# Kernel tuning notes

Hardware: AMD Instinct MI355X
Metric: run time of the kernel (lower is better)

The kernel has to match this reference:

```python
import jax, jax.numpy as jnp
import numpy as np

N = 100000      # n_entities + n_users (graph nodes)
E = 1600000     # edges
R = 8           # relations
D = 64          # entity_dim
DR = 64         # relation_dim
EPS = 1e-12


def setup_inputs() -> dict:
    key = jax.random.key(0)
    ks = jax.random.split(key, 16)
    inp = {
        'entity_emb': jax.random.normal(ks[0], (N, D), jnp.float32) * 0.1,
        'rel_emb':    jax.random.normal(ks[1], (R, DR), jnp.float32) * 0.1,
        'W_R':        jax.random.normal(ks[2], (R, D, DR), jnp.float32) * 0.1,
        'W1_0': jax.random.normal(ks[3], (32, 64), jnp.float32) * 0.1,
        'b1_0': jax.random.normal(ks[4], (32,), jnp.float32) * 0.1,
        'W2_0': jax.random.normal(ks[5], (32, 64), jnp.float32) * 0.1,
        'b2_0': jax.random.normal(ks[6], (32,), jnp.float32) * 0.1,
        'W1_1': jax.random.normal(ks[7], (16, 32), jnp.float32) * 0.1,
        'b1_1': jax.random.normal(ks[8], (16,), jnp.float32) * 0.1,
        'W2_1': jax.random.normal(ks[9], (16, 32), jnp.float32) * 0.1,
        'b2_1': jax.random.normal(ks[10], (16,), jnp.float32) * 0.1,
        'src':   jax.random.randint(ks[11], (E,), 0, N, dtype=jnp.int32),
        'dst':   jax.random.randint(ks[12], (E,), 0, N, dtype=jnp.int32),
        'etype': jax.random.randint(ks[13], (E,), 0, R, dtype=jnp.int32),
    }
    return inp


def _l2_normalize(x):
    # F.normalize(x, p=2, dim=1)
    n = jnp.linalg.norm(x, axis=1, keepdims=True)
    return x / jnp.maximum(n, EPS)


def reference(entity_emb, rel_emb, W_R, W1_0, b1_0, W2_0, b2_0,
              W1_1, b1_1, W2_1, b2_1, src, dst, etype):
    # ---- compute_attention: per-edge relation-specific projection ----
    # proj[n, r, :] = entity_emb[n] @ W_R[r]   -> [N, R, DR]
    proj = jnp.einsum('nd,rdk->nrk', entity_emb, W_R)
    r_mul_t = proj[src, etype]          # [E, DR] (edges.src)
    r_mul_h = proj[dst, etype]          # [E, DR] (edges.dst)
    r_e = rel_emb[etype]                # [E, DR]
    att = jnp.sum(r_mul_t * jnp.tanh(r_mul_h + r_e), axis=-1)  # [E]

    # ---- edge_softmax: normalize over incoming edges of each dst ----
    m = jax.ops.segment_max(att, dst, num_segments=N)           # [N]
    ex = jnp.exp(att - m[dst])
    s = jax.ops.segment_sum(ex, dst, num_segments=N)            # [N]
    a = ex / s[dst]                                             # [E]

    # ---- bi-interaction aggregator layers ----
    def agg_layer(x, W1, b1, W2, b2):
        msg = x[src] * a[:, None]                               # u_mul_e
        Nh = jax.ops.segment_sum(msg, dst, num_segments=N)      # sum to dst
        out1 = jax.nn.leaky_relu(jnp.matmul(x + Nh, W1.T) + b1, 0.01)
        out2 = jax.nn.leaky_relu(jnp.matmul(x * Nh, W2.T) + b2, 0.01)
        return _l2_normalize(out1 + out2)

    ego = entity_emb
    h1 = agg_layer(ego, W1_0, b1_0, W2_0, b2_0)   # [N, 32]
    h2 = agg_layer(h1, W1_1, b1_1, W2_1, b2_1)    # [N, 16]
    all_embed = jnp.concatenate([ego, h1, h2], axis=1)  # [N, 112]
    return all_embed
```

## Files before the change

### kernel.cpp

```cpp
#include <hip/hip_runtime.h>
#include <hip/hip_bf16.h>
#include <math.h>

#define NN 100000
#define NE 1600000
#define NR 8
#define DD 64
#define DDR 64

typedef __attribute__((ext_vector_type(8))) short bf8v;
typedef __attribute__((ext_vector_type(4))) float f4v;

__device__ __forceinline__ unsigned enc_f(float f) {
    unsigned u = __float_as_uint(f);
    return (u & 0x80000000u) ? ~u : (u | 0x80000000u);
}
__device__ __forceinline__ float dec_f(unsigned u) {
    return (u & 0x80000000u) ? __uint_as_float(u & 0x7FFFFFFFu) : __uint_as_float(~u);
}
__device__ __forceinline__ float bfs2f(unsigned short u) { return __uint_as_float(((unsigned)u) << 16); }
__device__ __forceinline__ short f2bfs(float x) {
    __hip_bfloat16 h = __float2bfloat16(x);
    return *reinterpret_cast<short*>(&h);
}
__device__ __forceinline__ unsigned pack2bf(short a, short b) {
    return (unsigned)(unsigned short)a | ((unsigned)(unsigned short)b << 16);
}
__device__ __forceinline__ float tanh_fast(float x) {
    x = fminf(fmaxf(x, -15.f), 15.f);
    float e = __expf(2.f * x);
    return (e - 1.f) * __builtin_amdgcn_rcpf(e + 1.f);
}

__global__ void __launch_bounds__(256)
k_projm(const float* __restrict__ emb, const float* __restrict__ WR,
        const float* __restrict__ rel,
        unsigned short* __restrict__ tproj, unsigned* __restrict__ embh)
{
    int t = threadIdx.x;
    int wv = t >> 6, l = t & 63;
    int lo = l & 15, hi = l >> 4;
    int r = blockIdx.y;
    int colbase = (wv & 1) * 32;
    int nwbase = blockIdx.x * 128 + (wv >> 1) * 64;

    const float* __restrict__ wb = WR + (long)r * (DD * DDR) + (hi * 8) * DDR + colbase + lo;
    bf8v B00, B01, B10, B11;
#pragma unroll
    for (int j = 0; j < 8; ++j) {
        B00[j] = f2bfs(wb[(0 * 32 + j) * DDR + 0]);
        B01[j] = f2bfs(wb[(1 * 32 + j) * DDR + 0]);
        B10[j] = f2bfs(wb[(0 * 32 + j) * DDR + 16]);
        B11[j] = f2bfs(wb[(1 * 32 + j) * DDR + 16]);
    }
    float rv0 = rel[r * DDR + colbase + lo];
    float rv1 = rel[r * DDR + colbase + lo + 16];

    for (int nt = 0; nt < 4; ++nt) {
        int nb = nwbase + nt * 16;
        int arow = nb + lo;
        float4 xa0 = make_float4(0.f, 0.f, 0.f, 0.f), xa1 = xa0, xb0 = xa0, xb1 = xa0;
        if (arow < NN) {
            const float* __restrict__ xr = emb + (long)arow * DD + hi * 8;
            xa0 = *(const float4*)(xr);
            xa1 = *(const float4*)(xr + 4);
            xb0 = *(const float4*)(xr + 32);
            xb1 = *(const float4*)(xr + 36);
        }
        bf8v A0, A1;
        A0[0] = f2bfs(xa0.x); A0[1] = f2bfs(xa0.y); A0[2] = f2bfs(xa0.z); A0[3] = f2bfs(xa0.w);
        A0[4] = f2bfs(xa1.x); A0[5] = f2bfs(xa1.y); A0[6] = f2bfs(xa1.z); A0[7] = f2bfs(xa1.w);
        A1[0] = f2bfs(xb0.x); A1[1] = f2bfs(xb0.y); A1[2] = f2bfs(xb0.z); A1[3] = f2bfs(xb0.w);
        A1[4] = f2bfs(xb1.x); A1[5] = f2bfs(xb1.y); A1[6] = f2bfs(xb1.z); A1[7] = f2bfs(xb1.w);

        if (r == 0 && arow < NN) {
            unsigned* er = embh + (long)arow * 32 + hi * 4;
            er[0]  = pack2bf(A0[0], A0[1]); er[1]  = pack2bf(A0[2], A0[3]);
            er[2]  = pack2bf(A0[4], A0[5]); er[3]  = pack2bf(A0[6], A0[7]);
            er[16] = pack2bf(A1[0], A1[1]); er[17] = pack2bf(A1[2], A1[3]);
            er[18] = pack2bf(A1[4], A1[5]); er[19] = pack2bf(A1[6], A1[7]);
        }

        f4v acc0 = {0.f, 0.f, 0.f, 0.f}, acc1 = {0.f, 0.f, 0.f, 0.f};
        acc0 = __builtin_amdgcn_mfma_f32_16x16x32_bf16(A0, B00, acc0, 0, 0, 0);
        acc0 = __builtin_amdgcn_mfma_f32_16x16x32_bf16(A1, B01, acc0, 0, 0, 0);
        acc1 = __builtin_amdgcn_mfma_f32_16x16x32_bf16(A0, B10, acc1, 0, 0, 0);
        acc1 = __builtin_amdgcn_mfma_f32_16x16x32_bf16(A1, B11, acc1, 0, 0, 0);

#pragma unroll
        for (int i = 0; i < 4; ++i) {
            int rr = nb + hi * 4 + i;
            if (rr < NN) {
                long obase = ((long)r * NN + rr) * DDR + colbase + lo;
                tproj[obase]      = (unsigned short)f2bfs(tanh_fast(acc0[i] + rv0));
                tproj[obase + 16] = (unsigned short)f2bfs(tanh_fast(acc1[i] + rv1));
            }
        }
    }
}

__global__ void __launch_bounds__(256)
k_projw2(const unsigned short* __restrict__ tproj, const float* __restrict__ WR,
         unsigned short* __restrict__ w2h)
{
    int t = threadIdx.x;
    int wv = t >> 6, l = t & 63;
    int lo = l & 15, hi = l >> 4;
    int r = blockIdx.y;
    int colbase = (wv & 1) * 32;
    int nwbase = blockIdx.x * 128 + (wv >> 1) * 64;

    const float* __restrict__ wb0 = WR + (long)r * (DD * DDR) + (long)(colbase + lo) * DDR + hi * 8;
    const float* __restrict__ wb1 = wb0 + 16 * DDR;
    bf8v B00, B01, B10, B11;
#pragma unroll
    for (int j = 0; j < 8; ++j) {
        B00[j] = f2bfs(wb0[j]);
        B01[j] = f2bfs(wb0[32 + j]);
        B10[j] = f2bfs(wb1[j]);
        B11[j] = f2bfs(wb1[32 + j]);
    }

    for (int nt = 0; nt < 4; ++nt) {
        int nb = nwbase + nt * 16;
        int arow = nb + lo;
        bf8v A0, A1;
#pragma unroll
        for (int j = 0; j < 8; ++j) { A0[j] = 0; A1[j] = 0; }
        if (arow < NN) {
            const unsigned short* ar = tproj + ((long)r * NN + arow) * DDR + hi * 8;
            A0 = *(const bf8v*)(ar);
            A1 = *(const bf8v*)(ar + 32);
        }
        f4v acc0 = {0.f, 0.f, 0.f, 0.f}, acc1 = {0.f, 0.f, 0.f, 0.f};
        acc0 = __builtin_amdgcn_mfma_f32_16x16x32_bf16(A0, B00, acc0, 0, 0, 0);
        acc0 = __builtin_amdgcn_mfma_f32_16x16x32_bf16(A1, B01, acc0, 0, 0, 0);
        acc1 = __builtin_amdgcn_mfma_f32_16x16x32_bf16(A0, B10, acc1, 0, 0, 0);
        acc1 = __builtin_amdgcn_mfma_f32_16x16x32_bf16(A1, B11, acc1, 0, 0, 0);
#pragma unroll
        for (int i = 0; i < 4; ++i) {
            int rr = nb + hi * 4 + i;
            if (rr < NN) {
                long obase = ((long)r * NN + rr) * DDR + colbase + lo;
                w2h[obase]      = (unsigned short)f2bfs(acc0[i]);
                w2h[obase + 16] = (unsigned short)f2bfs(acc1[i]);
            }
        }
    }
}

__global__ void k_hist(const int* __restrict__ dst, unsigned* __restrict__ cnt)
{
    int e = blockIdx.x * blockDim.x + threadIdx.x;
    if (e >= NE) return;
    atomicAdd(cnt + dst[e], 1u);
}

__global__ void k_base(const unsigned* __restrict__ cnt, unsigned* __restrict__ gcur,
                       unsigned* __restrict__ base, unsigned* __restrict__ curs)
{
    int i = blockIdx.x * blockDim.x + threadIdx.x;
    int lane = threadIdx.x & 63;
    unsigned v = (i < NN) ? cnt[i] : 0u;
    unsigned p = v;
#pragma unroll
    for (int off = 1; off < 64; off <<= 1) {
        unsigned q = __shfl_up(p, off);
        if (lane >= off) p += q;
    }
    unsigned tot = __shfl(p, 63);
    unsigned gb = 0;
    if (lane == 0) gb = atomicAdd(gcur, tot);
    gb = __shfl(gb, 0);
    if (i < NN) {
        unsigned b = gb + p - v;
        base[i] = b;
        curs[i] = b;
    }
}

__global__ void k_scatter2(const int* __restrict__ dst, const int* __restrict__ src,
                           const int* __restrict__ et, unsigned* __restrict__ curs,
                           unsigned* __restrict__ srcet)
{
    int e = blockIdx.x * blockDim.x + threadIdx.x;
    if (e >= NE) return;
    unsigned pos = atomicAdd(curs + dst[e], 1u);
    srcet[pos] = (unsigned)src[e] | ((unsigned)et[e] << 28);
}

__global__ void __launch_bounds__(256)
k_mega0w(const float* __restrict__ emb, const unsigned short* __restrict__ embh,
         const unsigned short* __restrict__ w2h,
         const unsigned* __restrict__ cnt, const unsigned* __restrict__ basep,
         const unsigned* __restrict__ srcet, float* __restrict__ acsr,
         unsigned short* __restrict__ h1h,
         const float* __restrict__ W1, const float* __restrict__ b1,
         const float* __restrict__ W2, const float* __restrict__ b2,
         float* __restrict__ out)
{
    __shared__ float W1T[64][33];
    __shared__ float W2T[64][33];
    __shared__ float sm1[4][64];
    __shared__ float sm2[4][64];
    int t = threadIdx.x;
#pragma unroll
    for (int i = 0; i < 8; ++i) {
        int idx = i * 256 + t;
        W1T[idx & 63][idx >> 6] = W1[idx];
        W2T[idx & 63][idx >> 6] = W2[idx];
    }
    int wv = t >> 6, lane = t & 63;
    int g = blockIdx.x * 4 + wv;
    int deg = (int)cnt[g];
    long b = basep[g];
    float Nh = 0.f;
    if (deg > 0 && deg <= 64) {
        float w0 = bfs2f(w2h[((long)0 * NN + g) * DDR + lane]);
        float w1_ = bfs2f(w2h[((long)1 * NN + g) * DDR + lane]);
        float w2_ = bfs2f(w2h[((long)2 * NN + g) * DDR + lane]);
        float w3 = bfs2f(w2h[((long)3 * NN + g) * DDR + lane]);
        float w4 = bfs2f(w2h[((long)4 * NN + g) * DDR + lane]);
        float w5 = bfs2f(w2h[((long)5 * NN + g) * DDR + lane]);
        float w6 = bfs2f(w2h[((long)6 * NN + g) * DDR + lane]);
        float w7 = bfs2f(w2h[((long)7 * NN + g) * DDR + lane]);
        unsigned se = 0;
        if (lane < deg) se = srcet[b + lane];
        float acc = 0.f, s_ = 0.f, myexp = 0.f;
        for (int i = 0; i < deg; i += 2) {
            int i1 = (i + 1 < deg) ? i + 1 : i;
            unsigned se0 = __shfl(se, i);
            unsigned se1 = __shfl(se, i1);
            int s0 = (int)(se0 & 0x0FFFFFFFu), r0 = (int)(se0 >> 28);
            int s1 = (int)(se1 & 0x0FFFFFFFu), r1 = (int)(se1 >> 28);
            float v0 = bfs2f(embh[(long)s0 * DD + lane]);
            float v1 = bfs2f(embh[(long)s1 * DD + lane]);
            float wa = (r0 & 4) ? ((r0 & 2) ? ((r0 & 1) ? w7 : w6) : ((r0 & 1) ? w5 : w4))
                                : ((r0 & 2) ? ((r0 & 1) ? w3 : w2_) : ((r0 & 1) ? w1_ : w0));
            float wbx = (r1 & 4) ? ((r1 & 2) ? ((r1 & 1) ? w7 : w6) : ((r1 & 1) ? w5 : w4))
                                 : ((r1 & 2) ? ((r1 & 1) ? w3 : w2_) : ((r1 & 1) ? w1_ : w0));
            float p0 = v0 * wa;
            float p1 = v1 * wbx;
#pragma unroll
            for (int off = 32; off; off >>= 1) {
                p0 += __shfl_xor(p0, off);
                p1 += __shfl_xor(p1, off);
            }
            float ex0 = __expf(fminf(p0, 60.f));
            float ex1 = (i + 1 < deg) ? __expf(fminf(p1, 60.f)) : 0.f;
            if (lane == i) myexp = ex0;
            if (lane == i + 1 && i + 1 < deg) myexp = ex1;
            s_ += ex0 + ex1;
            acc = fmaf(v0, ex0, fmaf(v1, ex1, acc));
        }
        float inv = 1.f / s_;
        if (lane < deg) acsr[b + lane] = myexp * inv;
        Nh = acc * inv;
    } else if (deg > 64) {
        float s_ = 0.f, acc = 0.f;
        for (int i = 0; i < deg; ++i) {
            unsigned sei = srcet[b + i];
            int s = (int)(sei & 0x0FFFFFFFu), r = (int)(sei >> 28);
            float v = bfs2f(embh[(long)s * DD + lane]);
            float wvl = bfs2f(w2h[((long)r * NN + g) * DDR + lane]);
            float p = v * wvl;
#pragma unroll
            for (int off = 32; off; off >>= 1) p += __shfl_xor(p, off);
            float ex = __expf(fminf(p, 60.f));
            s_ += ex;
            acc = fmaf(v, ex, acc);
            if (lane == 0) acsr[b + i] = ex;
        }
        float inv = 1.f / s_;
        for (int i = lane; i < deg; i += 64) acsr[b + i] *= inv;
        Nh = acc * inv;
    }
    float x = emb[(long)g * DD + lane];
    sm1[wv][lane] = x + Nh;
    sm2[wv][lane] = x * Nh;
    __syncthreads();
    int j = lane & 31;
    const float* __restrict__ WT = (lane < 32) ? &W1T[0][0] : &W2T[0][0];
    const float* __restrict__ sm = (lane < 32) ? &sm1[wv][0] : &sm2[wv][0];
    float accm = (lane < 32) ? b1[j] : b2[j];
#pragma unroll 8
    for (int dd = 0; dd < 64; ++dd)
        accm = fmaf(sm[dd], WT[dd * 33 + j], accm);
    accm = (accm >= 0.f) ? accm : 0.01f * accm;
    float other = __shfl_down(accm, 32);
    float h = accm + other;
    float ss = h * h;
#pragma unroll
    for (int off = 16; off; off >>= 1) ss += __shfl_xor(ss, off);
    float hn = h / fmaxf(sqrtf(ss), 1e-12f);
    out[(long)g * 112 + lane] = x;
    if (lane < 32) {
        out[(long)g * 112 + 64 + j] = hn;
        h1h[(long)g * 32 + j] = (unsigned short)f2bfs(hn);
    }
}

__global__ void __launch_bounds__(256)
k_mega1(const float* __restrict__ acsr, const unsigned* __restrict__ srcet,
        const unsigned* __restrict__ cnt, const unsigned* __restrict__ basep,
        const unsigned short* __restrict__ h1h,
        const float* __restrict__ W1, const float* __restrict__ b1,
        const float* __restrict__ W2, const float* __restrict__ b2,
        float* __restrict__ out)
{
    __shared__ float W1T[32][17];
    __shared__ float W2T[32][17];
    __shared__ float sm1[8][32];
    __shared__ float sm2[8][32];
    int t = threadIdx.x;
#pragma unroll
    for (int i = 0; i < 2; ++i) {
        int idx = i * 256 + t;
        W1T[idx & 31][idx >> 5] = W1[idx];
        W2T[idx & 31][idx >> 5] = W2[idx];
    }
    int grp = t >> 5, l5 = t & 31;
    int g = blockIdx.x * 8 + grp;
    int deg = (int)cnt[g];
    float acc = 0.f;
    if (deg > 0) {
        long b = basep[g];
        unsigned se = 0; float a = 0.f;
        if (l5 < deg) { se = srcet[b + l5]; a = acsr[b + l5]; }
        int dmin = (deg < 32) ? deg : 32;
        int i = 0;
        for (; i + 1 < dmin; i += 2) {
            float a0 = __shfl(a, i, 32), a1 = __shfl(a, i + 1, 32);
            int s0 = (int)(__shfl(se, i, 32) & 0x0FFFFFFFu);
            int s1 = (int)(__shfl(se, i + 1, 32) & 0x0FFFFFFFu);
            float v0 = bfs2f(h1h[(long)s0 * 32 + l5]);
            float v1 = bfs2f(h1h[(long)s1 * 32 + l5]);
            acc = fmaf(v0, a0, acc);
            acc = fmaf(v1, a1, acc);
        }
        if (i < dmin) {
            float a0 = __shfl(a, i, 32);
            int s0 = (int)(__shfl(se, i, 32) & 0x0FFFFFFFu);
            acc = fmaf(bfs2f(h1h[(long)s0 * 32 + l5]), a0, acc);
        }
        for (int k = 32; k < deg; ++k) {
            float ak = acsr[b + k];
            int sk = (int)(srcet[b + k] & 0x0FFFFFFFu);
            acc = fmaf(bfs2f(h1h[(long)sk * 32 + l5]), ak, acc);
        }
    }
    float x = out[(long)g * 112 + 64 + l5];
    sm1[grp][l5] = x + acc;
    sm2[grp][l5] = x * acc;
    __syncthreads();
    int j = l5 & 15;
    const float* __restrict__ WT = (l5 < 16) ? &W1T[0][0] : &W2T[0][0];
    const float* __restrict__ sm = (l5 < 16) ? &sm1[grp][0] : &sm2[grp][0];
    float accm = (l5 < 16) ? b1[j] : b2[j];
#pragma unroll 8
    for (int dd = 0; dd < 32; ++dd)
        accm = fmaf(sm[dd], WT[dd * 17 + j], accm);
    accm = (accm >= 0.f) ? accm : 0.01f * accm;
    float other = __shfl_down(accm, 16, 32);
    float h = accm + other;
    float ss = h * h;
#pragma unroll
    for (int off = 8; off; off >>= 1) ss += __shfl_xor(ss, off);
    float hn = h / fmaxf(sqrtf(ss), 1e-12f);
    if (l5 < 16) out[(long)g * 112 + 96 + j] = hn;
}

__global__ void k_att(const float* __restrict__ emb, const float* __restrict__ rel,
                      const float* __restrict__ WR, const int* __restrict__ src,
                      const int* __restrict__ dst, const int* __restrict__ et,
                      float* __restrict__ att, unsigned* __restrict__ mkey)
{
    int e = (int)((blockIdx.x * blockDim.x + threadIdx.x) >> 6);
    int lane = threadIdx.x & 63;
    if (e >= NE) return;
    int s = src[e], d = dst[e], r = et[e];
    const float* __restrict__ es = emb + (long)s * DD;
    const float* __restrict__ eh = emb + (long)d * DD;
    const float* __restrict__ w  = WR + r * (DD * DDR) + lane;
    float at = 0.f, ah = 0.f;
#pragma unroll 8
    for (int dd = 0; dd < DD; ++dd) {
        float ws = w[dd * DDR];
        at = fmaf(es[dd], ws, at);
        ah = fmaf(eh[dd], ws, ah);
    }
    float term = at * tanhf(ah + rel[r * DDR + lane]);
#pragma unroll
    for (int off = 32; off; off >>= 1) term += __shfl_xor(term, off);
    if (lane == 0) {
        att[e] = term;
        atomicMax(mkey + d, enc_f(term));
    }
}

__global__ void k_expsum(const int* __restrict__ dst, float* __restrict__ att,
                         const unsigned* __restrict__ mkey, float* __restrict__ ssum)
{
    int e = blockIdx.x * blockDim.x + threadIdx.x;
    if (e >= NE) return;
    int d = dst[e];
    float ex = expf(att[e] - dec_f(mkey[d]));
    att[e] = ex;
    atomicAdd(ssum + d, ex);
}

__global__ void k_agg0(const float* __restrict__ emb, const int* __restrict__ src,
                       const int* __restrict__ dst, float* __restrict__ att,
                       const float* __restrict__ ssum, float* __restrict__ Nh)
{
    int e = (int)((blockIdx.x * blockDim.x + threadIdx.x) >> 6);
    int lane = threadIdx.x & 63;
    if (e >= NE) return;
    int s = src[e], d = dst[e];
    float a = att[e] / ssum[d];
    if (lane == 0) att[e] = a;
    float v = emb[(long)s * DD + lane] * a;
    atomicAdd(Nh + (long)d * DD + lane, v);
}

__global__ void k_agg1(const float* __restrict__ out, const int* __restrict__ src,
                       const int* __restrict__ dst, const float* __restrict__ att,
                       float* __restrict__ Nh1)
{
    int idx = blockIdx.x * blockDim.x + threadIdx.x;
    int e = idx >> 5;
    int j = idx & 31;
    if (e >= NE) return;
    int s = src[e], d = dst[e];
    float a = att[e];
    float v = out[(long)s * 112 + 64 + j] * a;
    atomicAdd(Nh1 + (long)d * 32 + j, v);
}

#define NPB0 32
__global__ void __launch_bounds__(256)
k_node0t(const float* __restrict__ emb, const float* __restrict__ Nh,
         const float* __restrict__ W1, const float* __restrict__ b1,
         const float* __restrict__ W2, const float* __restrict__ b2,
         float* __restrict__ out)
{
    __shared__ float W1T[64][33];
    __shared__ float W2T[64][33];
    int t = threadIdx.x;
#pragma unroll
    for (int i = 0; i < 8; ++i) {
        int idx = i * 256 + t;
        W1T[idx & 63][idx >> 6] = W1[idx];
        W2T[idx & 63][idx >> 6] = W2[idx];
    }
    __syncthreads();
    int wv = t >> 6, lane = t & 63, j = lane & 31;
    const float* __restrict__ WT = (lane < 32) ? &W1T[0][0] : &W2T[0][0];
    float bj = (lane < 32) ? b1[j] : b2[j];
    int n0 = blockIdx.x * NPB0;
    int n1 = (n0 + NPB0 < NN) ? n0 + NPB0 : NN;
    for (int node = n0 + wv; node < n1; node += 4) {
        const float* __restrict__ x  = emb + (long)node * DD;
        const float* __restrict__ nh = Nh + (long)node * DD;
        float acc = 0.f;
#pragma unroll 8
        for (int dd = 0; dd < DD; ++dd) {
            float xv = x[dd], nv = nh[dd];
            float v = (lane < 32) ? (xv + nv) : (xv * nv);
            acc = fmaf(v, WT[dd * 33 + j], acc);
        }
        acc += bj;
        acc = (acc >= 0.f) ? acc : 0.01f * acc;
        float other = __shfl_down(acc, 32);
        float h = acc + other;
        float ss = h * h;
#pragma unroll
        for (int off = 16; off; off >>= 1) ss += __shfl_xor(ss, off);
        float hn = h / fmaxf(sqrtf(ss), 1e-12f);
        out[(long)node * 112 + lane] = x[lane];
        if (lane < 32) out[(long)node * 112 + 64 + j] = hn;
    }
}

#define NPB1 32
__global__ void __launch_bounds__(256)
k_node1t(const float* __restrict__ outbuf, const float* __restrict__ Nh1,
         const float* __restrict__ W1, const float* __restrict__ b1,
         const float* __restrict__ W2, const float* __restrict__ b2,
         float* __restrict__ out)
{
    __shared__ float W1T[32][17];
    __shared__ float W2T[32][17];
    int t = threadIdx.x;
#pragma unroll
    for (int i = 0; i < 2; ++i) {
        int idx = i * 256 + t;
        W1T[idx & 31][idx >> 5] = W1[idx];
        W2T[idx & 31][idx >> 5] = W2[idx];
    }
    __syncthreads();
    int grp = t >> 5;
    int l5 = t & 31, j = l5 & 15;
    const float* __restrict__ WT = (l5 < 16) ? &W1T[0][0] : &W2T[0][0];
    float bj = (l5 < 16) ? b1[j] : b2[j];
    int n0 = blockIdx.x * NPB1;
    int n1 = (n0 + NPB1 < NN) ? n0 + NPB1 : NN;
    for (int node = n0 + grp; node < n1; node += 8) {
        const float* __restrict__ x  = outbuf + (long)node * 112 + 64;
        const float* __restrict__ nh = Nh1 + (long)node * 32;
        float acc = 0.f;
#pragma unroll 8
        for (int dd = 0; dd < 32; ++dd) {
            float xv = x[dd], nv = nh[dd];
            float v = (l5 < 16) ? (xv + nv) : (xv * nv);
            acc = fmaf(v, WT[dd * 17 + j], acc);
        }
        acc += bj;
        acc = (acc >= 0.f) ? acc : 0.01f * acc;
        float other = __shfl_down(acc, 16, 32);
        float h = acc + other;
        float ss = h * h;
#pragma unroll
        for (int off = 8; off; off >>= 1) ss += __shfl_xor(ss, off);
        float hn = h / fmaxf(sqrtf(ss), 1e-12f);
        if (l5 < 16) out[(long)node * 112 + 96 + j] = hn;
    }
}

extern "C" void kernel_launch(void* const* d_in, const int* in_sizes, int n_in,
                              void* d_out, int out_size, void* d_ws, size_t ws_size,
                              hipStream_t stream) {
    const float* emb  = (const float*)d_in[0];
    const float* rel  = (const float*)d_in[1];
    const float* WR   = (const float*)d_in[2];
    const float* W1_0 = (const float*)d_in[3];
    const float* b1_0 = (const float*)d_in[4];
    const float* W2_0 = (const float*)d_in[5];
    const float* b2_0 = (const float*)d_in[6];
    const float* W1_1 = (const float*)d_in[7];
    const float* b1_1 = (const float*)d_in[8];
    const float* W2_1 = (const float*)d_in[9];
    const float* b2_1 = (const float*)d_in[10];
    const int*   src  = (const int*)d_in[11];
    const int*   dst  = (const int*)d_in[12];
    const int*   et   = (const int*)d_in[13];
    float* out = (float*)d_out;

    unsigned* cnt   = (unsigned*)d_ws;
    unsigned* gcur  = cnt + NN;
    unsigned* basep = cnt + NN + 64;
    unsigned* curs  = cnt + 2 * NN + 64;
    float* acsr  = (float*)d_ws + 3 * NN + 64;
    unsigned* srcet = (unsigned*)(acsr + NE);
    unsigned short* tproj = (unsigned short*)(srcet + NE);
    unsigned short* w2h = tproj + (size_t)NR * NN * DDR;
    unsigned* embh = (unsigned*)(w2h + (size_t)NR * NN * DDR);
    unsigned short* h1h = (unsigned short*)(embh + (size_t)NN * 32);

    size_t need = ((size_t)3 * NN + 64 + 2 * (size_t)NE) * 4
                + 2 * (size_t)NR * NN * DDR * 2
                + (size_t)NN * 32 * 4 + (size_t)NN * 16 * 4;

    if (ws_size >= need) {
        hipMemsetAsync(d_ws, 0, (size_t)(NN + 64) * sizeof(unsigned), stream);
        k_hist<<<dim3((NE + 255) / 256), dim3(256), 0, stream>>>(dst, cnt);
        k_projm<<<dim3((NN + 127) / 128, NR), dim3(256), 0, stream>>>(
            emb, WR, rel, tproj, embh);
        k_projw2<<<dim3((NN + 127) / 128, NR), dim3(256), 0, stream>>>(
            tproj, WR, w2h);
        k_base<<<dim3((NN + 255) / 256), dim3(256), 0, stream>>>(cnt, gcur, basep, curs);
        k_scatter2<<<dim3((NE + 255) / 256), dim3(256), 0, stream>>>(
            dst, src, et, curs, srcet);
        k_mega0w<<<dim3((NN + 3) / 4), dim3(256), 0, stream>>>(
            emb, (const unsigned short*)embh, w2h, cnt, basep, srcet, acsr, h1h,
            W1_0, b1_0, W2_0, b2_0, out);
        k_mega1<<<dim3((NN + 7) / 8), dim3(256), 0, stream>>>(
            acsr, srcet, cnt, basep, h1h, W1_1, b1_1, W2_1, b2_1, out);
    } else {
        unsigned* mkey = (unsigned*)d_ws;
        float* ssum = (float*)d_ws + NN;
        float* fNh0 = (float*)d_ws + 2 * NN;
        float* fNh1 = (float*)d_ws + (2 + DD) * NN;
        float* fatt = (float*)d_ws + (2 + DD + 32) * NN;
        hipMemsetAsync(d_ws, 0, (size_t)(2 + DD + 32) * NN * sizeof(float), stream);
        k_att<<<dim3((int)(((long)NE * 64 + 255) / 256)), dim3(256), 0, stream>>>(
            emb, rel, WR, src, dst, et, fatt, mkey);
        k_expsum<<<dim3((NE + 255) / 256), dim3(256), 0, stream>>>(dst, fatt, mkey, ssum);
        k_agg0<<<dim3((int)(((long)NE * 64 + 255) / 256)), dim3(256), 0, stream>>>(
            emb, src, dst, fatt, ssum, fNh0);
        k_node0t<<<dim3((NN + NPB0 - 1) / NPB0), dim3(256), 0, stream>>>(
            emb, fNh0, W1_0, b1_0, W2_0, b2_0, out);
        k_agg1<<<dim3((int)(((long)NE * 32 + 255) / 256)), dim3(256), 0, stream>>>(
            out, src, dst, fatt, fNh1);
        k_node1t<<<dim3((NN + NPB1 - 1) / NPB1), dim3(256), 0, stream>>>(
            out, fNh1, W1_1, b1_1, W2_1, b2_1, out);
    }
}
```

Before: 544.3 us.

## Split layer-0 attention into 4-edges-per-wave dot pass then aggregation pass

The per-node attention loop now computes scores for four edges at once, with 16 lanes per edge each loading a packed uint2 of bf16 values, instead of one edge per full-wave reduction. Scores are staged in shared memory, and a proper max-subtracted softmax is computed across the wave before a separate pass aggregates neighbour embeddings. This shortens the shuffle-reduction chain and drops the eight per-relation register preloads and the select tree. The cost is that each source embedding row is read a second time in the aggregation pass, and the high-degree path becomes a three-pass loop.

```diff
diff --git a/kernel.cpp b/kernel.cpp
--- a/kernel.cpp
+++ b/kernel.cpp
@@ -18,6 +18,8 @@
 __device__ __forceinline__ float dec_f(unsigned u) {
     return (u & 0x80000000u) ? __uint_as_float(u & 0x7FFFFFFFu) : __uint_as_float(~u);
 }
+__device__ __forceinline__ float bflo(unsigned u) { return __uint_as_float(u << 16); }
+__device__ __forceinline__ float bfhi(unsigned u) { return __uint_as_float(u & 0xFFFF0000u); }
 __device__ __forceinline__ float bfs2f(unsigned short u) { return __uint_as_float(((unsigned)u) << 16); }
 __device__ __forceinline__ short f2bfs(float x) {
     __hip_bfloat16 h = __float2bfloat16(x);
@@ -190,19 +192,20 @@
 }
 
 __global__ void __launch_bounds__(256)
-k_mega0w(const float* __restrict__ emb, const unsigned short* __restrict__ embh,
-         const unsigned short* __restrict__ w2h,
-         const unsigned* __restrict__ cnt, const unsigned* __restrict__ basep,
-         const unsigned* __restrict__ srcet, float* __restrict__ acsr,
-         unsigned short* __restrict__ h1h,
-         const float* __restrict__ W1, const float* __restrict__ b1,
-         const float* __restrict__ W2, const float* __restrict__ b2,
-         float* __restrict__ out)
+k_mega0(const float* __restrict__ emb, const unsigned* __restrict__ embh,
+        const unsigned* __restrict__ w2h,
+        const unsigned* __restrict__ cnt, const unsigned* __restrict__ basep,
+        const unsigned* __restrict__ srcet, float* __restrict__ acsr,
+        unsigned short* __restrict__ h1h,
+        const float* __restrict__ W1, const float* __restrict__ b1,
+        const float* __restrict__ W2, const float* __restrict__ b2,
+        float* __restrict__ out)
 {
     __shared__ float W1T[64][33];
     __shared__ float W2T[64][33];
     __shared__ float sm1[4][64];
     __shared__ float sm2[4][64];
+    __shared__ float att_s[4][64];
     int t = threadIdx.x;
 #pragma unroll
     for (int i = 0; i < 8; ++i) {
@@ -215,65 +218,79 @@
     int deg = (int)cnt[g];
     long b = basep[g];
     float Nh = 0.f;
+    const unsigned short* embh_us = (const unsigned short*)embh;
     if (deg > 0 && deg <= 64) {
-        float w0 = bfs2f(w2h[((long)0 * NN + g) * DDR + lane]);
-        float w1_ = bfs2f(w2h[((long)1 * NN + g) * DDR + lane]);
-        float w2_ = bfs2f(w2h[((long)2 * NN + g) * DDR + lane]);
-        float w3 = bfs2f(w2h[((long)3 * NN + g) * DDR + lane]);
-        float w4 = bfs2f(w2h[((long)4 * NN + g) * DDR + lane]);
-        float w5 = bfs2f(w2h[((long)5 * NN + g) * DDR + lane]);
-        float w6 = bfs2f(w2h[((long)6 * NN + g) * DDR + lane]);
-        float w7 = bfs2f(w2h[((long)7 * NN + g) * DDR + lane]);
         unsigned se = 0;
         if (lane < deg) se = srcet[b + lane];
-        float acc = 0.f, s_ = 0.f, myexp = 0.f;
-        for (int i = 0; i < deg; i += 2) {
-            int i1 = (i + 1 < deg) ? i + 1 : i;
-            unsigned se0 = __shfl(se, i);
-            unsigned se1 = __shfl(se, i1);
-            int s0 = (int)(se0 & 0x0FFFFFFFu), r0 = (int)(se0 >> 28);
-            int s1 = (int)(se1 & 0x0FFFFFFFu), r1 = (int)(se1 >> 28);
-            float v0 = bfs2f(embh[(long)s0 * DD + lane]);
-            float v1 = bfs2f(embh[(long)s1 * DD + lane]);
-            float wa = (r0 & 4) ? ((r0 & 2) ? ((r0 & 1) ? w7 : w6) : ((r0 & 1) ? w5 : w4))
-                                : ((r0 & 2) ? ((r0 & 1) ? w3 : w2_) : ((r0 & 1) ? w1_ : w0));
-            float wbx = (r1 & 4) ? ((r1 & 2) ? ((r1 & 1) ? w7 : w6) : ((r1 & 1) ? w5 : w4))
-                                 : ((r1 & 2) ? ((r1 & 1) ? w3 : w2_) : ((r1 & 1) ? w1_ : w0));
-            float p0 = v0 * wa;
-            float p1 = v1 * wbx;
-#pragma unroll
-            for (int off = 32; off; off >>= 1) {
-                p0 += __shfl_xor(p0, off);
-                p1 += __shfl_xor(p1, off);
-            }
-            float ex0 = __expf(fminf(p0, 60.f));
-            float ex1 = (i + 1 < deg) ? __expf(fminf(p1, 60.f)) : 0.f;
-            if (lane == i) myexp = ex0;
-            if (lane == i + 1 && i + 1 < deg) myexp = ex1;
-            s_ += ex0 + ex1;
-            acc = fmaf(v0, ex0, fmaf(v1, ex1, acc));
-        }
+        int gi = lane >> 4;
+        int lj = lane & 15;
+        for (int k0 = 0; k0 < deg; k0 += 4) {
+            int ei = k0 + gi;
+            unsigned sei = __shfl(se, ei);
+            int s = (int)(sei & 0x0FFFFFFFu);
+            int r = (int)(sei >> 28);
+            uint2 tv = *(const uint2*)(embh + (long)s * 32 + lj * 2);
+            uint2 hv = *(const uint2*)(w2h + ((long)r * NN + g) * 32 + lj * 2);
+            float sum = bflo(tv.x) * bflo(hv.x) + bfhi(tv.x) * bfhi(hv.x)
+                      + bflo(tv.y) * bflo(hv.y) + bfhi(tv.y) * bfhi(hv.y);
+#pragma unroll
+            for (int off = 8; off; off >>= 1) sum += __shfl_xor(sum, off);
+            if (lj == 0 && ei < deg) att_s[wv][ei] = sum;
+        }
+        float attv = (lane < deg) ? att_s[wv][lane] : -3.4e38f;
+        float m = attv;
+#pragma unroll
+        for (int off = 32; off; off >>= 1) m = fmaxf(m, __shfl_xor(m, off));
+        float exv = (lane < deg) ? __expf(attv - m) : 0.f;
+        float s_ = exv;
+#pragma unroll
+        for (int off = 32; off; off >>= 1) s_ += __shfl_xor(s_, off);
         float inv = 1.f / s_;
-        if (lane < deg) acsr[b + lane] = myexp * inv;
+        if (lane < deg) acsr[b + lane] = exv * inv;
+        float acc = 0.f;
+        int i = 0;
+        for (; i + 1 < deg; i += 2) {
+            float a0 = __shfl(exv, i), a1 = __shfl(exv, i + 1);
+            int s0 = (int)(__shfl(se, i) & 0x0FFFFFFFu);
+            int s1 = (int)(__shfl(se, i + 1) & 0x0FFFFFFFu);
+            float v0 = bfs2f(embh_us[(long)s0 * DD + lane]);
+            float v1 = bfs2f(embh_us[(long)s1 * DD + lane]);
+            acc = fmaf(v0, a0, acc);
+            acc = fmaf(v1, a1, acc);
+        }
+        if (i < deg) {
+            float a0 = __shfl(exv, i);
+            int s0 = (int)(__shfl(se, i) & 0x0FFFFFFFu);
+            acc = fmaf(bfs2f(embh_us[(long)s0 * DD + lane]), a0, acc);
+        }
         Nh = acc * inv;
     } else if (deg > 64) {
-        float s_ = 0.f, acc = 0.f;
+        float m = -3.4e38f;
         for (int i = 0; i < deg; ++i) {
             unsigned sei = srcet[b + i];
             int s = (int)(sei & 0x0FFFFFFFu), r = (int)(sei >> 28);
-            float v = bfs2f(embh[(long)s * DD + lane]);
-            float wvl = bfs2f(w2h[((long)r * NN + g) * DDR + lane]);
+            float v = bfs2f(embh_us[(long)s * DD + lane]);
+            float wvl = bfs2f(((const unsigned short*)w2h)[((long)r * NN + g) * DDR + lane]);
             float p = v * wvl;
 #pragma unroll
             for (int off = 32; off; off >>= 1) p += __shfl_xor(p, off);
-            float ex = __expf(fminf(p, 60.f));
-            s_ += ex;
-            acc = fmaf(v, ex, acc);
-            if (lane == 0) acsr[b + i] = ex;
-        }
+            if (lane == 0) acsr[b + i] = p;
+            m = fmaxf(m, p);
+        }
+        float s_ = 0.f;
+        for (int i = lane; i < deg; i += 64) s_ += __expf(acsr[b + i] - m);
+#pragma unroll
+        for (int off = 32; off; off >>= 1) s_ += __shfl_xor(s_, off);
         float inv = 1.f / s_;
-        for (int i = lane; i < deg; i += 64) acsr[b + i] *= inv;
-        Nh = acc * inv;
+        float acc = 0.f;
+        for (int i = 0; i < deg; ++i) {
+            float raw = acsr[b + i];
+            float a = __expf(raw - m) * inv;
+            int s = (int)(srcet[b + i] & 0x0FFFFFFFu);
+            acc = fmaf(bfs2f(embh_us[(long)s * DD + lane]), a, acc);
+            if (lane == 0) acsr[b + i] = a;
+        }
+        Nh = acc;
     }
     float x = emb[(long)g * DD + lane];
     sm1[wv][lane] = x + Nh;
@@ -567,12 +584,12 @@
         k_projm<<<dim3((NN + 127) / 128, NR), dim3(256), 0, stream>>>(
             emb, WR, rel, tproj, embh);
         k_projw2<<<dim3((NN + 127) / 128, NR), dim3(256), 0, stream>>>(
-            tproj, WR, w2h);
+            tproj, WR, (unsigned short*)w2h);
         k_base<<<dim3((NN + 255) / 256), dim3(256), 0, stream>>>(cnt, gcur, basep, curs);
         k_scatter2<<<dim3((NE + 255) / 256), dim3(256), 0, stream>>>(
             dst, src, et, curs, srcet);
-        k_mega0w<<<dim3((NN + 3) / 4), dim3(256), 0, stream>>>(
-            emb, (const unsigned short*)embh, w2h, cnt, basep, srcet, acsr, h1h,
+        k_mega0<<<dim3((NN + 3) / 4), dim3(256), 0, stream>>>(
+            emb, embh, (const unsigned*)w2h, cnt, basep, srcet, acsr, h1h,
             W1_0, b1_0, W2_0, b2_0, out);
         k_mega1<<<dim3((NN + 7) / 8), dim3(256), 0, stream>>>(
             acsr, srcet, cnt, basep, h1h, W1_1, b1_1, W2_1, b2_1, out);
```

Result: no change. 536.5 us (-1.4%).
